# Performance work log

Hardware: AMD Instinct MI355X
Metric: run time of the kernel (lower is better)

Reference implementation:

```python
import jax, jax.numpy as jnp
import numpy as np


def _depthwise3x3(x_nhwc, w):
    # w: (3, 3, 1, C) — depthwise conv, padding=1, matches torch Conv2d(groups=C)
    return jax.lax.conv_general_dilated(
        x_nhwc, w, window_strides=(1, 1), padding='SAME',
        dimension_numbers=('NHWC', 'HWIO', 'NHWC'),
        feature_group_count=x_nhwc.shape[-1])


def _stripe_attn(q, k, v, lepe_w, B, H, W, nh, hd, ss, axis, scale):
    # q/k/v: (B, H, W, nh*hd); axis 0 = horizontal stripes, 1 = vertical
    pad_h = (-H) % ss if axis == 0 else 0
    pad_w = (-W) % ss if axis == 1 else 0
    if pad_h or pad_w:
        pad = ((0, 0), (0, pad_h), (0, pad_w), (0, 0))
        q, k, v = jnp.pad(q, pad), jnp.pad(k, pad), jnp.pad(v, pad)
    Hp, Wp = q.shape[1], q.shape[2]
    lepe = _depthwise3x3(v, lepe_w)  # (B, Hp, Wp, nh*hd)

    if axis == 0:
        nS = Hp // ss
        def to_win(t):  # -> (B*nS*Wp, nh, ss, hd)
            t = t.reshape(B, nS, ss, Wp, nh, hd)
            return t.transpose(0, 1, 3, 4, 2, 5).reshape(B * nS * Wp, nh, ss, hd)
    else:
        nS = Wp // ss
        def to_win(t):  # -> (B*Hp*nS, nh, ss, hd)
            t = t.reshape(B, Hp, nS, ss, nh, hd)
            return t.transpose(0, 1, 2, 4, 3, 5).reshape(B * Hp * nS, nh, ss, hd)

    qw, kw, vw, lw = to_win(q), to_win(k), to_win(v), to_win(lepe)
    attn = jax.nn.softmax(jnp.einsum('wnqd,wnkd->wnqk', qw, kw) / scale, axis=-1)
    out = jnp.einsum('wnqk,wnkd->wnqd', attn, vw) + lw  # (Wnum, nh, ss, hd)

    if axis == 0:
        out = out.transpose(0, 2, 1, 3).reshape(B, nS, Wp, ss, nh * hd)
        out = out.transpose(0, 1, 3, 2, 4).reshape(B, Hp, Wp, nh * hd)
    else:
        out = out.transpose(0, 2, 1, 3).reshape(B, Hp, nS, ss, nh * hd)
        out = out.reshape(B, Hp, Wp, nh * hd)
    return out[:, :H, :W, :].reshape(B, H * W, nh * hd)


def setup_inputs() -> dict:
    key = jax.random.key(0)
    ks = jax.random.split(key, 6)
    B, H, W, dim, n_heads, ss = 8, 64, 64, 512, 16, 8
    half = dim // 2
    x = jax.random.normal(ks[0], (B, H * W, dim), dtype=jnp.float32)
    w_qkv = jax.random.normal(ks[1], (3 * dim, dim), dtype=jnp.float32) * 0.02
    w_proj = jax.random.normal(ks[2], (dim, dim), dtype=jnp.float32) * 0.02
    b_proj = jnp.zeros((dim,), dtype=jnp.float32)
    lepe_h_w = jax.random.normal(ks[3], (3, 3, 1, half), dtype=jnp.float32) * 0.1
    lepe_v_w = jax.random.normal(ks[4], (3, 3, 1, half), dtype=jnp.float32) * 0.1
    return {"x": x, "w_qkv": w_qkv, "w_proj": w_proj, "b_proj": b_proj,
            "lepe_h_w": lepe_h_w, "lepe_v_w": lepe_v_w, "H": H, "W": W}


def reference(x, w_qkv, w_proj, b_proj, lepe_h_w, lepe_v_w, H, W):
    B, L, C = x.shape
    n_heads, ss = 16, 8
    hd = C // n_heads
    scale = float(np.sqrt(hd))
    qkv = x @ w_qkv.T  # (B, L, 3C)
    q, k, v = jnp.split(qkv, 3, axis=-1)
    q = q.reshape(B, H, W, C)
    k = k.reshape(B, H, W, C)
    v = v.reshape(B, H, W, C)
    half = C // 2
    nh_h = n_heads // 2
    nh_v = n_heads - nh_h
    out_h = _stripe_attn(q[..., :half], k[..., :half], v[..., :half],
                         lepe_h_w, B, H, W, nh_h, hd, ss, axis=0, scale=scale)
    out_v = _stripe_attn(q[..., half:], k[..., half:], v[..., half:],
                         lepe_v_w, B, H, W, nh_v, hd, ss, axis=1, scale=scale)
    out = jnp.concatenate([out_h, out_v], axis=-1)
    return out @ w_proj.T + b_proj
```

## Files before the change

### kernel.cpp

```cpp
#include <hip/hip_runtime.h>
#include <hip/hip_bf16.h>
#include <stdint.h>

typedef _Float16 half2v __attribute__((ext_vector_type(2)));
typedef _Float16 half8v __attribute__((ext_vector_type(8)));
typedef uint32_t u32x4  __attribute__((ext_vector_type(4)));
typedef float    f32x4  __attribute__((ext_vector_type(4)));

__device__ __forceinline__ unsigned short f2h(float f) {
  _Float16 h = (_Float16)f;
  return __builtin_bit_cast(unsigned short, h);
}
__device__ __forceinline__ half2v bch2(uint32_t u) {
  return __builtin_bit_cast(half2v, u);
}
__device__ __forceinline__ uint32_t pkrtz_u32(float a, float b) {
  return __builtin_bit_cast(uint32_t, __builtin_amdgcn_cvt_pkrtz(a, b));
}

__device__ __forceinline__ int qkv_idx(int half, int b, int n, int h, int w) {
  int idx = half * 8388608 + (b * 8 + n) * 131072;
  idx += (half == 0) ? ((h >> 3) * 16384 + w * 256 + (h & 7) * 32)
                     : (h * 2048 + w * 32);
  return idx;
}

#define GLOAD_LDS16(gsrc, lbase)                                          \
  __builtin_amdgcn_global_load_lds(                                       \
      (const __attribute__((address_space(1))) uint32_t*)(gsrc),          \
      (__attribute__((address_space(3))) uint32_t*)(lbase), 16, 0, 0)

__global__ __launch_bounds__(256) void cvt_f32_f16(const float* __restrict__ in,
                                                   unsigned short* __restrict__ out,
                                                   int n4) {
  int i = blockIdx.x * 256 + threadIdx.x;
  if (i >= n4) return;
  float4 f = reinterpret_cast<const float4*>(in)[i];
  ushort4 u;
  u.x = f2h(f.x); u.y = f2h(f.y); u.z = f2h(f.z); u.w = f2h(f.w);
  reinterpret_cast<ushort4*>(out)[i] = u;
}

template<int MODE>
__global__ __launch_bounds__(256) void gemm_bt(
    const unsigned short* __restrict__ A,
    const unsigned short* __restrict__ B,
    unsigned short* __restrict__ Cq,
    float* __restrict__ Cf,
    const float* __restrict__ bias,
    int M, int N, int K)
{
  __shared__ unsigned short As[2][128 * 32];
  __shared__ unsigned short Bs[2][128 * 32];
  const int tid  = threadIdx.x;
  const int m0   = blockIdx.x * 128;
  const int n0   = blockIdx.y * 128;
  const int wave = tid >> 6, lane = tid & 63;
  const int wr = wave >> 1, wc = wave & 1;
  const int sr = tid >> 2;
  const int sc = ((tid & 3) ^ ((tid >> 3) & 3)) * 8;
  const size_t aBase0 = (size_t)(m0 + sr) * K + sc;
  const size_t aBase1 = (size_t)(m0 + 64 + sr) * K + sc;
  const size_t bBase0 = (size_t)(n0 + sr) * K + sc;
  const size_t bBase1 = (size_t)(n0 + 64 + sr) * K + sc;
  char* ldsA = (char*)(&As[0][0]) + (tid & ~63) * 16;
  char* ldsB = (char*)(&Bs[0][0]) + (tid & ~63) * 16;

#define STAGE_TILE(bsel, kofs)                                  \
  do {                                                          \
    GLOAD_LDS16(A + aBase0 + (kofs), ldsA + (bsel) * 8192);     \
    GLOAD_LDS16(A + aBase1 + (kofs), ldsA + (bsel) * 8192 + 4096); \
    GLOAD_LDS16(B + bBase0 + (kofs), ldsB + (bsel) * 8192);     \
    GLOAD_LDS16(B + bBase1 + (kofs), ldsB + (bsel) * 8192 + 4096); \
  } while (0)

  STAGE_TILE(0, 0);

  f32x4 acc[4][4];
  const f32x4 zero = {0.f, 0.f, 0.f, 0.f};
  #pragma unroll
  for (int i = 0; i < 4; ++i)
    #pragma unroll
    for (int j = 0; j < 4; ++j) acc[i][j] = zero;

  const int lr   = lane & 15;
  const int slot = (lane >> 4) ^ ((lr >> 1) & 3);

  auto compute = [&](const unsigned short* Asb, const unsigned short* Bsb) {
    half8v af[4], bfr[4];
    #pragma unroll
    for (int i = 0; i < 4; ++i)
      af[i] = *reinterpret_cast<const half8v*>(Asb + (wr * 64 + i * 16 + lr) * 32 + slot * 8);
    #pragma unroll
    for (int j = 0; j < 4; ++j)
      bfr[j] = *reinterpret_cast<const half8v*>(Bsb + (wc * 64 + j * 16 + lr) * 32 + slot * 8);
    __builtin_amdgcn_s_setprio(1);
    #pragma unroll
    for (int i = 0; i < 4; ++i)
      #pragma unroll
      for (int j = 0; j < 4; ++j)
        acc[i][j] = __builtin_amdgcn_mfma_f32_16x16x32_f16(bfr[j], af[i], acc[i][j], 0, 0, 0);
    __builtin_amdgcn_s_setprio(0);
  };

  const int nt = K >> 5;
  for (int t = 0; t < nt - 1; ++t) {
    STAGE_TILE((t + 1) & 1, (t + 1) * 32);
    asm volatile("s_waitcnt vmcnt(4)" ::: "memory");
    __builtin_amdgcn_s_barrier();
    __builtin_amdgcn_sched_barrier(0);
    compute(&As[t & 1][0], &Bs[t & 1][0]);
    __builtin_amdgcn_s_barrier();
    __builtin_amdgcn_sched_barrier(0);
  }
  asm volatile("s_waitcnt vmcnt(0)" ::: "memory");
  __builtin_amdgcn_s_barrier();
  __builtin_amdgcn_sched_barrier(0);
  compute(&As[(nt - 1) & 1][0], &Bs[(nt - 1) & 1][0]);
#undef STAGE_TILE

  const int cr = (lane >> 4) * 4;
  const int cc = lane & 15;

  if constexpr (MODE == 0) {
    #pragma unroll
    for (int j = 0; j < 4; ++j) {
      const int n = n0 + wc * 64 + j * 16 + cr;
      const float4 b4 = *reinterpret_cast<const float4*>(bias + n);
      #pragma unroll
      for (int i = 0; i < 4; ++i) {
        const int m = m0 + wr * 64 + i * 16 + cc;
        float4 r;
        r.x = acc[i][j][0] + b4.x;
        r.y = acc[i][j][1] + b4.y;
        r.z = acc[i][j][2] + b4.z;
        r.w = acc[i][j][3] + b4.w;
        *reinterpret_cast<float4*>(Cf + (size_t)m * N + n) = r;
      }
    }
  } else {
    const int mb   = m0 + wr * 64;
    const int btok = mb >> 12;
    const int htok = (mb >> 6) & 63;
    #pragma unroll
    for (int j = 0; j < 4; ++j) {
      const int nb    = n0 + wc * 64 + j * 16 + cr;
      const int tq    = nb >> 9;
      const int halfc = (nb >> 8) & 1;
      const int nn    = (nb & 255) >> 5;
      const int ch4   = nb & 31;
      int base = tq * 16777216 + halfc * 8388608 + (btok * 8 + nn) * 131072 + ch4;
      base += halfc ? (htok * 2048) : ((htok >> 3) * 16384 + (htok & 7) * 32);
      const int wstride = halfc ? 32 : 256;
      #pragma unroll
      for (int i = 0; i < 4; ++i) {
        const int wpix = i * 16 + cc;
        uint2 r;
        r.x = pkrtz_u32(acc[i][j][0], acc[i][j][1]);
        r.y = pkrtz_u32(acc[i][j][2], acc[i][j][3]);
        *reinterpret_cast<uint2*>(Cq + base + wpix * wstride) = r;
      }
    }
  }
}

__global__ __launch_bounds__(256) void attn_lepe(
    const unsigned short* __restrict__ qkvp,
    const unsigned short* __restrict__ wlep,
    unsigned short* __restrict__ outp)
{
  const int gw   = (int)((blockIdx.x * 256 + threadIdx.x) >> 6);
  const int lane = threadIdx.x & 63;
  const int half = gw >> 15;
  const int id   = gw & 32767;
  const int b    = id >> 12;
  const int n    = (id >> 9) & 7;
  int h0, w0;
  if (half == 0) { const int s = (id >> 6) & 7; h0 = s * 8; w0 = id & 63; }
  else           { const int s = id & 7; h0 = (id >> 3) & 63; w0 = s * 8; }
  const int winbase = qkv_idx(half, b, n, h0, w0);
  const unsigned short* qwin = qkvp + winbase;
  const unsigned short* kwin = qkvp + 16777216 + winbase;
  const unsigned short* vwin = qkvp + 33554432 + winbase;

  const int qr = lane >> 3, kr = lane & 7;
  const unsigned short* qp = qwin + qr * 32;
  const unsigned short* kp = kwin + kr * 32;
  float s_val = 0.f;
  #pragma unroll
  for (int c = 0; c < 4; ++c) {
    u32x4 qv = *reinterpret_cast<const u32x4*>(qp + c * 8);
    u32x4 kv = *reinterpret_cast<const u32x4*>(kp + c * 8);
    #pragma unroll
    for (int e = 0; e < 4; ++e)
      s_val = __builtin_amdgcn_fdot2(bch2(qv[e]), bch2(kv[e]), s_val, false);
  }
  s_val *= 0.17677669529663687f;

  float p = __expf(s_val);
  float den = p;
  den += __shfl_xor(den, 1);
  den += __shfl_xor(den, 2);
  den += __shfl_xor(den, 4);
  const float a = p * __builtin_amdgcn_rcpf(den);
  const _Float16 ah = (_Float16)a;
  half2v ad = {ah, ah};
  const uint32_t adu = __builtin_bit_cast(uint32_t, ad);

  const int d0 = (lane & 7) * 4;
  const int gb = lane & 56;
  half2v o01 = {0, 0}, o23 = {0, 0};
  #pragma unroll
  for (int k = 0; k < 8; ++k) {
    const half2v ak2 = bch2((uint32_t)__shfl((int)adu, gb | k));
    const uint2 vv = *reinterpret_cast<const uint2*>(vwin + k * 32 + d0);
    o01 += ak2 * bch2(vv.x);
    o23 += ak2 * bch2(vv.y);
  }

  const int hq = h0 + ((half == 0) ? qr : 0);
  const int wq = w0 + ((half == 0) ? 0 : qr);
  const unsigned short* vplane = qkvp + 33554432;
  const unsigned short* wl = wlep + half * 2304 + n * 32 + d0;
  half2v l01 = {0, 0}, l23 = {0, 0};
  #pragma unroll
  for (int dy = -1; dy <= 1; ++dy) {
    #pragma unroll
    for (int dx = -1; dx <= 1; ++dx) {
      const int hh = hq + dy, ww = wq + dx;
      uint2 vv; vv.x = 0u; vv.y = 0u;
      if ((unsigned)hh < 64u && (unsigned)ww < 64u)
        vv = *reinterpret_cast<const uint2*>(vplane + qkv_idx(half, b, n, hh, ww) + d0);
      const uint2 wt = *reinterpret_cast<const uint2*>(wl + ((dy + 1) * 3 + dx + 1) * 256);
      l01 += bch2(wt.x) * bch2(vv.x);
      l23 += bch2(wt.y) * bch2(vv.y);
    }
  }

  const int m = b * 4096 + hq * 64 + wq;
  const int chan0 = half * 256 + n * 32;
  const half2v r01 = o01 + l01;
  const half2v r23 = o23 + l23;
  uint2 r;
  r.x = __builtin_bit_cast(uint32_t, r01);
  r.y = __builtin_bit_cast(uint32_t, r23);
  *reinterpret_cast<uint2*>(outp + (size_t)m * 512 + chan0 + d0) = r;
}

extern "C" void kernel_launch(void* const* d_in, const int* in_sizes, int n_in,
                              void* d_out, int out_size, void* d_ws, size_t ws_size,
                              hipStream_t stream) {
  const float* x      = (const float*)d_in[0];
  const float* w_qkv  = (const float*)d_in[1];
  const float* w_proj = (const float*)d_in[2];
  const float* b_proj = (const float*)d_in[3];
  const float* lepe_h = (const float*)d_in[4];
  const float* lepe_v = (const float*)d_in[5];
  float* out = (float*)d_out;

  char* ws = (char*)d_ws;
  unsigned short* qkv_p   = (unsigned short*)ws;
  unsigned short* xh      = (unsigned short*)(ws + 100663296);
  unsigned short* wqkv_h  = (unsigned short*)(ws + 134217728);
  unsigned short* wproj_h = (unsigned short*)(ws + 135790592);
  unsigned short* wlep_h  = (unsigned short*)(ws + 136314880);

  cvt_f32_f16<<<16384, 256, 0, stream>>>(x, xh, 4194304);
  cvt_f32_f16<<<768,   256, 0, stream>>>(w_qkv, wqkv_h, 196608);
  cvt_f32_f16<<<256,   256, 0, stream>>>(w_proj, wproj_h, 65536);
  cvt_f32_f16<<<3,     256, 0, stream>>>(lepe_h, wlep_h, 576);
  cvt_f32_f16<<<3,     256, 0, stream>>>(lepe_v, wlep_h + 2304, 576);

  gemm_bt<1><<<dim3(256, 12), 256, 0, stream>>>(
      xh, wqkv_h, qkv_p, nullptr, nullptr, 32768, 1536, 512);

  attn_lepe<<<16384, 256, 0, stream>>>(qkv_p, wlep_h, xh);

  gemm_bt<0><<<dim3(256, 4), 256, 0, stream>>>(
      xh, wproj_h, nullptr, out, b_proj, 32768, 512, 512);
}
```

Before: 208.0 us.

## Process two stripe windows per wave and swap GEMM grid axes for locality

After: 194.3 us. 6.6% less time.

```diff
diff --git a/kernel.cpp b/kernel.cpp
--- a/kernel.cpp
+++ b/kernel.cpp
@@ -53,8 +53,8 @@
   __shared__ unsigned short As[2][128 * 32];
   __shared__ unsigned short Bs[2][128 * 32];
   const int tid  = threadIdx.x;
-  const int m0   = blockIdx.x * 128;
-  const int n0   = blockIdx.y * 128;
+  const int m0   = blockIdx.y * 128;
+  const int n0   = blockIdx.x * 128;
   const int wave = tid >> 6, lane = tid & 63;
   const int wr = wave >> 1, wc = wave & 1;
   const int sr = tid >> 2;
@@ -171,80 +171,93 @@
 {
   const int gw   = (int)((blockIdx.x * 256 + threadIdx.x) >> 6);
   const int lane = threadIdx.x & 63;
-  const int half = gw >> 15;
-  const int id   = gw & 32767;
-  const int b    = id >> 12;
-  const int n    = (id >> 9) & 7;
+  const int half = gw >> 14;
+  const int id   = gw & 16383;
+  const int b    = id >> 11;
+  const int n    = (id >> 8) & 7;
   int h0, w0;
-  if (half == 0) { const int s = (id >> 6) & 7; h0 = s * 8; w0 = id & 63; }
-  else           { const int s = id & 7; h0 = (id >> 3) & 63; w0 = s * 8; }
-  const int winbase = qkv_idx(half, b, n, h0, w0);
-  const unsigned short* qwin = qkvp + winbase;
-  const unsigned short* kwin = qkvp + 16777216 + winbase;
-  const unsigned short* vwin = qkvp + 33554432 + winbase;
+  if (half == 0) { h0 = ((id >> 5) & 7) * 8; w0 = (id & 31) * 2; }
+  else           { h0 = ((id >> 3) & 31) * 2; w0 = (id & 7) * 8; }
+  const int baseA = qkv_idx(half, b, n, h0, w0);
+  const int dWin  = (half == 0) ? 256 : 2048;
+  const int baseB = baseA + dWin;
 
   const int qr = lane >> 3, kr = lane & 7;
-  const unsigned short* qp = qwin + qr * 32;
-  const unsigned short* kp = kwin + kr * 32;
-  float s_val = 0.f;
+  const unsigned short* qA = qkvp + baseA + qr * 32;
+  const unsigned short* kA = qkvp + 16777216 + baseA + kr * 32;
+  float sA = 0.f, sB = 0.f;
   #pragma unroll
   for (int c = 0; c < 4; ++c) {
-    u32x4 qv = *reinterpret_cast<const u32x4*>(qp + c * 8);
-    u32x4 kv = *reinterpret_cast<const u32x4*>(kp + c * 8);
-    #pragma unroll
-    for (int e = 0; e < 4; ++e)
-      s_val = __builtin_amdgcn_fdot2(bch2(qv[e]), bch2(kv[e]), s_val, false);
-  }
-  s_val *= 0.17677669529663687f;
-
-  float p = __expf(s_val);
-  float den = p;
-  den += __shfl_xor(den, 1);
-  den += __shfl_xor(den, 2);
-  den += __shfl_xor(den, 4);
-  const float a = p * __builtin_amdgcn_rcpf(den);
-  const _Float16 ah = (_Float16)a;
-  half2v ad = {ah, ah};
-  const uint32_t adu = __builtin_bit_cast(uint32_t, ad);
-
-  const int d0 = (lane & 7) * 4;
-  const int gb = lane & 56;
-  half2v o01 = {0, 0}, o23 = {0, 0};
+    const u32x4 qa = *reinterpret_cast<const u32x4*>(qA + c * 8);
+    const u32x4 ka = *reinterpret_cast<const u32x4*>(kA + c * 8);
+    const u32x4 qb = *reinterpret_cast<const u32x4*>(qA + dWin + c * 8);
+    const u32x4 kb = *reinterpret_cast<const u32x4*>(kA + dWin + c * 8);
+    #pragma unroll
+    for (int e = 0; e < 4; ++e) {
+      sA = __builtin_amdgcn_fdot2(bch2(qa[e]), bch2(ka[e]), sA, false);
+      sB = __builtin_amdgcn_fdot2(bch2(qb[e]), bch2(kb[e]), sB, false);
+    }
+  }
+  const float scl = 0.17677669529663687f;
+  const float pA = __expf(sA * scl);
+  const float pB = __expf(sB * scl);
+  float denA = pA, denB = pB;
+  denA += __shfl_xor(denA, 1); denA += __shfl_xor(denA, 2); denA += __shfl_xor(denA, 4);
+  denB += __shfl_xor(denB, 1); denB += __shfl_xor(denB, 2); denB += __shfl_xor(denB, 4);
+  const float aAv = pA * __builtin_amdgcn_rcpf(denA);
+  const float aBv = pB * __builtin_amdgcn_rcpf(denB);
+  const uint32_t adu = pkrtz_u32(aAv, aBv);
+
+  const int dgrp = lane & 3;
+  const int win  = (lane >> 2) & 1;
+  const int qr2  = lane >> 3;
+  const int d0   = dgrp * 8;
+  const int mybase = win ? baseB : baseA;
+  const unsigned short* vwin = qkvp + 33554432 + mybase;
+
+  half2v o01 = {0,0}, o23 = {0,0}, o45 = {0,0}, o67 = {0,0};
   #pragma unroll
   for (int k = 0; k < 8; ++k) {
-    const half2v ak2 = bch2((uint32_t)__shfl((int)adu, gb | k));
-    const uint2 vv = *reinterpret_cast<const uint2*>(vwin + k * 32 + d0);
-    o01 += ak2 * bch2(vv.x);
-    o23 += ak2 * bch2(vv.y);
-  }
-
-  const int hq = h0 + ((half == 0) ? qr : 0);
-  const int wq = w0 + ((half == 0) ? 0 : qr);
+    const uint32_t pairw = (uint32_t)__shfl((int)adu, qr2 * 8 + k);
+    const half2v ph = bch2(pairw);
+    const _Float16 av = win ? ph.y : ph.x;
+    const half2v ak2 = {av, av};
+    const u32x4 vv = *reinterpret_cast<const u32x4*>(vwin + k * 32 + d0);
+    o01 += ak2 * bch2(vv[0]);
+    o23 += ak2 * bch2(vv[1]);
+    o45 += ak2 * bch2(vv[2]);
+    o67 += ak2 * bch2(vv[3]);
+  }
+
+  const int hq = (half == 0) ? (h0 + qr2) : (h0 + win);
+  const int wq = (half == 0) ? (w0 + win) : (w0 + qr2);
   const unsigned short* vplane = qkvp + 33554432;
   const unsigned short* wl = wlep + half * 2304 + n * 32 + d0;
-  half2v l01 = {0, 0}, l23 = {0, 0};
+  half2v l01 = {0,0}, l23 = {0,0}, l45 = {0,0}, l67 = {0,0};
   #pragma unroll
   for (int dy = -1; dy <= 1; ++dy) {
     #pragma unroll
     for (int dx = -1; dx <= 1; ++dx) {
       const int hh = hq + dy, ww = wq + dx;
-      uint2 vv; vv.x = 0u; vv.y = 0u;
+      u32x4 vv = {0u, 0u, 0u, 0u};
       if ((unsigned)hh < 64u && (unsigned)ww < 64u)
-        vv = *reinterpret_cast<const uint2*>(vplane + qkv_idx(half, b, n, hh, ww) + d0);
-      const uint2 wt = *reinterpret_cast<const uint2*>(wl + ((dy + 1) * 3 + dx + 1) * 256);
-      l01 += bch2(wt.x) * bch2(vv.x);
-      l23 += bch2(wt.y) * bch2(vv.y);
+        vv = *reinterpret_cast<const u32x4*>(vplane + qkv_idx(half, b, n, hh, ww) + d0);
+      const u32x4 wt = *reinterpret_cast<const u32x4*>(wl + ((dy + 1) * 3 + dx + 1) * 256);
+      l01 += bch2(wt[0]) * bch2(vv[0]);
+      l23 += bch2(wt[1]) * bch2(vv[1]);
+      l45 += bch2(wt[2]) * bch2(vv[2]);
+      l67 += bch2(wt[3]) * bch2(vv[3]);
     }
   }
 
   const int m = b * 4096 + hq * 64 + wq;
   const int chan0 = half * 256 + n * 32;
-  const half2v r01 = o01 + l01;
-  const half2v r23 = o23 + l23;
-  uint2 r;
-  r.x = __builtin_bit_cast(uint32_t, r01);
-  r.y = __builtin_bit_cast(uint32_t, r23);
-  *reinterpret_cast<uint2*>(outp + (size_t)m * 512 + chan0 + d0) = r;
+  u32x4 r;
+  r[0] = __builtin_bit_cast(uint32_t, (half2v)(o01 + l01));
+  r[1] = __builtin_bit_cast(uint32_t, (half2v)(o23 + l23));
+  r[2] = __builtin_bit_cast(uint32_t, (half2v)(o45 + l45));
+  r[3] = __builtin_bit_cast(uint32_t, (half2v)(o67 + l67));
+  *reinterpret_cast<u32x4*>(outp + (size_t)m * 512 + chan0 + d0) = r;
 }
 
 extern "C" void kernel_launch(void* const* d_in, const int* in_sizes, int n_in,
@@ -271,11 +284,11 @@
   cvt_f32_f16<<<3,     256, 0, stream>>>(lepe_h, wlep_h, 576);
   cvt_f32_f16<<<3,     256, 0, stream>>>(lepe_v, wlep_h + 2304, 576);
 
-  gemm_bt<1><<<dim3(256, 12), 256, 0, stream>>>(
+  gemm_bt<1><<<dim3(12, 256), 256, 0, stream>>>(
       xh, wqkv_h, qkv_p, nullptr, nullptr, 32768, 1536, 512);
 
-  attn_lepe<<<16384, 256, 0, stream>>>(qkv_p, wlep_h, xh);
-
-  gemm_bt<0><<<dim3(256, 4), 256, 0, stream>>>(
+  attn_lepe<<<8192, 256, 0, stream>>>(qkv_p, wlep_h, xh);
+
+  gemm_bt<0><<<dim3(4, 256), 256, 0, stream>>>(
       xh, wproj_h, nullptr, out, b_proj, 32768, 512, 512);
 }
```
